# Performance work log

Measured on AMD Instinct MI355X. Metric: run time of the kernel, lower is better.

The kernel has to match this reference:

```python
import jax, jax.numpy as jnp
import numpy as np

B, N, T, E = 8, 10000, 12, 160000
C_IN, C_SP, C_OUT, K = 32, 64, 64, 3
EPS = 1e-5

def _conv1xk(x, w, b, pad):
    # x: (B, Cin, N, T), w: (Cout, Cin, 1, k) -- conv only along time axis
    y = jax.lax.conv_general_dilated(x, w, (1, 1), [(0, 0), (pad, pad)],
                                     dimension_numbers=('NCHW', 'OIHW', 'NCHW'))
    return y + b[None, :, None, None]

def _temporal_block(x, w, b, gamma, beta, mean, var):
    out = _conv1xk(x, w, b, pad=1)
    p, q = jnp.split(out, 2, axis=1)
    out = p * jax.nn.sigmoid(q)  # GLU gate
    scale = gamma * jax.lax.rsqrt(var + EPS)  # eval-mode BatchNorm2d
    return (out - mean[None, :, None, None]) * scale[None, :, None, None] + beta[None, :, None, None]

def _cheb_conv(x, edge_index, edge_weight, W, b):
    # x: (BT, N, C). PyG ChebConv, sym normalization, lambda_max=2 =>
    # Lhat = -D^{-1/2} A D^{-1/2} (zero diagonal). Recursion T0=x, T1=Lhat x,
    # Tk = 2 Lhat T_{k-1} - T_{k-2}; out = sum_k Tk @ W_k + b.
    row, col = edge_index[0], edge_index[1]
    n = x.shape[1]
    deg = jnp.zeros((n,), x.dtype).at[row].add(edge_weight)
    deg_safe = jnp.where(deg > 0, deg, 1.0)
    dinv = jnp.where(deg > 0, jax.lax.rsqrt(deg_safe), 0.0)
    norm = -edge_weight * dinv[row] * dinv[col]  # (E,)

    def lhat(z):
        msg = z[:, row, :] * norm[None, :, None]          # gather + scale
        return jnp.zeros_like(z).at[:, col, :].add(msg)   # scatter-add

    Tx0 = x
    out = jnp.einsum('bnc,cd->bnd', Tx0, W[0])
    Tx1 = lhat(x)
    out = out + jnp.einsum('bnc,cd->bnd', Tx1, W[1])
    for k in range(2, W.shape[0]):
        Tx2 = 2.0 * lhat(Tx1) - Tx0
        out = out + jnp.einsum('bnc,cd->bnd', Tx2, W[k])
        Tx0, Tx1 = Tx1, Tx2
    return out + b

def setup_inputs():
    key = jax.random.key(0)
    ks = jax.random.split(key, 16)
    s = 0.05
    return {
        'x': jax.random.normal(ks[0], (B, C_IN, N, T), jnp.float32),
        'edge_index': jax.random.randint(ks[1], (2, E), 0, N),
        'edge_weight': jax.random.uniform(ks[2], (E,), jnp.float32),
        'w_gate1': jax.random.normal(ks[3], (2 * C_SP, C_IN, 1, 3), jnp.float32) * s,
        'b_gate1': jnp.zeros((2 * C_SP,), jnp.float32),
        'bn1_gamma': 1.0 + 0.1 * jax.random.normal(ks[4], (C_SP,), jnp.float32),
        'bn1_beta': 0.1 * jax.random.normal(ks[5], (C_SP,), jnp.float32),
        'bn1_mean': 0.1 * jax.random.normal(ks[6], (C_SP,), jnp.float32),
        'bn1_var': jax.random.uniform(ks[7], (C_SP,), jnp.float32, 0.5, 1.5),
        'cheb_w': jax.random.normal(ks[8], (K, C_SP, C_SP), jnp.float32) * s,
        'cheb_b': jnp.zeros((C_SP,), jnp.float32),
        'ln_gamma': jnp.ones((C_SP,), jnp.float32),
        'ln_beta': jnp.zeros((C_SP,), jnp.float32),
        'w_gate2': jax.random.normal(ks[9], (2 * C_OUT, C_SP, 1, 3), jnp.float32) * s,
        'b_gate2': jnp.zeros((2 * C_OUT,), jnp.float32),
        'bn2_gamma': 1.0 + 0.1 * jax.random.normal(ks[10], (C_OUT,), jnp.float32),
        'bn2_beta': 0.1 * jax.random.normal(ks[11], (C_OUT,), jnp.float32),
        'bn2_mean': 0.1 * jax.random.normal(ks[12], (C_OUT,), jnp.float32),
        'bn2_var': jax.random.uniform(ks[13], (C_OUT,), jnp.float32, 0.5, 1.5),
        'w_res': jax.random.normal(ks[14], (C_OUT, C_IN, 1, 1), jnp.float32) * s,
        'b_res': jnp.zeros((C_OUT,), jnp.float32),
    }

def reference(x, edge_index, edge_weight, w_gate1, b_gate1, bn1_gamma, bn1_beta, bn1_mean, bn1_var,
              cheb_w, cheb_b, ln_gamma, ln_beta, w_gate2, b_gate2, bn2_gamma, bn2_beta, bn2_mean,
              bn2_var, w_res, b_res):
    b_, _, n_, t_ = x.shape
    res = _conv1xk(x, w_res, b_res, pad=0)  # 1x1 residual projection
    out = _temporal_block(x, w_gate1, b_gate1, bn1_gamma, bn1_beta, bn1_mean, bn1_var)
    c_s = out.shape[1]
    # (B, C_s, N, T) -> (B*T, N, C_s): spatial graph conv per time snapshot
    h = out.transpose(0, 3, 2, 1).reshape(b_ * t_, n_, c_s)
    h = _cheb_conv(h, edge_index, edge_weight, cheb_w, cheb_b)
    mu = h.mean(-1, keepdims=True)
    var = ((h - mu) ** 2).mean(-1, keepdims=True)
    h = (h - mu) * jax.lax.rsqrt(var + EPS) * ln_gamma + ln_beta  # LayerNorm
    h = jax.nn.relu(h)
    h = h.reshape(b_, t_, n_, c_s).transpose(0, 3, 2, 1)
    out = _temporal_block(h, w_gate2, b_gate2, bn2_gamma, bn2_beta, bn2_mean, bn2_var)
    return out + res
```

## Files before the change

### kernel.cpp

```cpp
#include <hip/hip_runtime.h>
#include <math.h>

#define BB 8
#define CIN 32
#define NN 10000
#define TTT 12
#define EE 160000
#define CSP 64
#define BT (BB*TTT)
#define EPSV 1e-5f

typedef __attribute__((ext_vector_type(8))) short bf16x8;
typedef __attribute__((ext_vector_type(4))) float f32x4;

static __device__ __forceinline__ float sigmoidf_(float v) {
    return __builtin_amdgcn_rcpf(1.f + __expf(-v));
}

static __device__ __forceinline__ short f2bf(float v) {
    unsigned u = __float_as_uint(v);
    u = (u + 0x7fffu + ((u >> 16) & 1u)) >> 16;
    return (short)u;
}
static __device__ __forceinline__ float lo16f(unsigned u) {
    return __uint_as_float(u << 16);
}
static __device__ __forceinline__ float hi16f(unsigned u) {
    return __uint_as_float(u & 0xffff0000u);
}
static __device__ __forceinline__ unsigned packbf(float a, float b) {
    return ((unsigned)(ushort)f2bf(a)) | (((unsigned)(ushort)f2bf(b)) << 16);
}

__global__ void k_deg(const int* __restrict__ ei, const float* __restrict__ ew,
                      float* __restrict__ deg) {
    int e = blockIdx.x * 256 + threadIdx.x;
    if (e < EE) atomicAdd(&deg[ei[e]], ew[e]);
}

__global__ void k_dinv(float* __restrict__ deg) {
    int n = blockIdx.x * 256 + threadIdx.x;
    if (n < NN) { float d = deg[n]; deg[n] = d > 0.f ? rsqrtf(d) : 0.f; }
}

__global__ void k_norm_cnt(const int* __restrict__ ei, const float* __restrict__ ew,
                           const float* __restrict__ dinv, float* __restrict__ nrm,
                           int* __restrict__ cnt) {
    int e = blockIdx.x * 256 + threadIdx.x;
    if (e < EE) {
        int r = ei[e], c = ei[EE + e];
        nrm[e] = -ew[e] * dinv[r] * dinv[c];
        atomicAdd(&cnt[c], 1);
    }
}

__global__ void k_scan(const int* __restrict__ cnt, int* __restrict__ offs,
                       int* __restrict__ cursor) {
    __shared__ int sh[1024];
    int tid = threadIdx.x;
    int running = 0;
    for (int base = 0; base < NN; base += 1024) {
        int i = base + tid;
        int v = (i < NN) ? cnt[i] : 0;
        sh[tid] = v;
        __syncthreads();
        for (int off = 1; off < 1024; off <<= 1) {
            int t = (tid >= off) ? sh[tid - off] : 0;
            __syncthreads();
            sh[tid] += t;
            __syncthreads();
        }
        int incl = sh[tid];
        if (i < NN) { offs[i] = running + incl - v; cursor[i] = running + incl - v; }
        int ct = sh[1023];
        __syncthreads();
        running += ct;
    }
    if (tid == 0) offs[NN] = running;
}

__global__ void k_fill(const int* __restrict__ ei, const float* __restrict__ nrm,
                       int* __restrict__ cursor, unsigned* __restrict__ csrp) {
    int e = blockIdx.x * 256 + threadIdx.x;
    if (e < EE) {
        int cdst = ei[EE + e];
        int p = atomicAdd(&cursor[cdst], 1);
        csrp[p] = (((unsigned)(ushort)f2bf(nrm[e])) << 16) | (unsigned)ei[e];
    }
}

__global__ void k_cvt_w(const float* __restrict__ wg1, const float* __restrict__ wg2,
                        const float* __restrict__ wr, const float* __restrict__ cwf,
                        short* __restrict__ o1, short* __restrict__ o2,
                        short* __restrict__ o3, short* __restrict__ wt02,
                        short* __restrict__ wt1, short* __restrict__ wt2) {
    int i = blockIdx.x * 256 + threadIdx.x;
    if (i < 12288) o1[i] = f2bf(wg1[i]);
    if (i < 24576) o2[i] = f2bf(wg2[i]);
    if (i < 2048)  o3[i] = f2bf(wr[i]);
    if (i < 4096) {
        int cout = i >> 6, cin = i & 63;
        float w0 = cwf[cin * 64 + cout];
        float w1 = cwf[4096 + cin * 64 + cout];
        float w2 = cwf[8192 + cin * 64 + cout];
        wt02[i] = f2bf(w0 - w2);
        wt1[i]  = f2bf(w1);
        wt2[i]  = f2bf(w2);
    }
}

__global__ __launch_bounds__(256, 4) void k_tconv1_mfma(
    const float* __restrict__ x, const short* __restrict__ wbf,
    const float* __restrict__ bg, const float* __restrict__ gam,
    const float* __restrict__ bet, const float* __restrict__ mean,
    const float* __restrict__ var, ushort* __restrict__ h1)
{
    __shared__ short Btl[3 * 48 * 40];
    int bi = blockIdx.x;
    int b = bi / 2500;
    int n0 = (bi % 2500) * 4;
    int tid = threadIdx.x;

    for (int j = tid; j < 384; j += 256) {
        int ci = j / 12, r = j - ci * 12;
        const float* xp = x + ((size_t)(b * CIN + ci) * NN + n0) * 12 + r * 4;
        float4 v = *(const float4*)xp;
        float vv[4] = {v.x, v.y, v.z, v.w};
#pragma unroll
        for (int e = 0; e < 4; ++e) {
            int at = r * 4 + e;
            int n = at / 12, t = at - n * 12;
            short bv = f2bf(vv[e]);
#pragma unroll
            for (int kk = 0; kk < 3; ++kk) {
                int tp = t + 1 - kk;
                if (tp >= 0 && tp < 12) {
                    int K = ci * 3 + kk;
                    Btl[((K >> 5) * 48 + n * 12 + tp) * 40 + (K & 31)] = bv;
                }
            }
            if (t == 0)  { int K = ci * 3;     Btl[((K >> 5) * 48 + n * 12) * 40 + (K & 31)] = 0; }
            if (t == 11) { int K = ci * 3 + 2; Btl[((K >> 5) * 48 + n * 12 + 11) * 40 + (K & 31)] = 0; }
        }
    }
    __syncthreads();

    int w = tid >> 6, l = tid & 63, lr = l & 15, lq = l >> 4;
    f32x4 aP[3], aQ[3];
#pragma unroll
    for (int m = 0; m < 3; ++m) { aP[m] = (f32x4){0,0,0,0}; aQ[m] = (f32x4){0,0,0,0}; }

#pragma unroll
    for (int ks = 0; ks < 3; ++ks) {
        bf16x8 wp = *(const bf16x8*)(wbf + ((w * 16 + lr) * 96 + ks * 32 + lq * 8));
        bf16x8 wq = *(const bf16x8*)(wbf + ((64 + w * 16 + lr) * 96 + ks * 32 + lq * 8));
#pragma unroll
        for (int mt = 0; mt < 3; ++mt) {
            bf16x8 im = *(const bf16x8*)(&Btl[(ks * 48 + mt * 16 + lr) * 40 + lq * 8]);
            aP[mt] = __builtin_amdgcn_mfma_f32_16x16x32_bf16(im, wp, aP[mt], 0, 0, 0);
            aQ[mt] = __builtin_amdgcn_mfma_f32_16x16x32_bf16(im, wq, aQ[mt], 0, 0, 0);
        }
    }

    int c = w * 16 + lr;
    float bp = bg[c], bq = bg[64 + c];
    float sc = gam[c] * rsqrtf(var[c] + EPSV);
    float mn = mean[c], be = bet[c];
#pragma unroll
    for (int mt = 0; mt < 3; ++mt) {
#pragma unroll
        for (int j = 0; j < 4; ++j) {
            int row = mt * 16 + lq * 4 + j;
            int n = n0 + row / 12, t = row % 12;
            float h = (aP[mt][j] + bp) * sigmoidf_(aQ[mt][j] + bq);
            h1[((size_t)(b * TTT + t) * NN + n) * 64 + c] = (ushort)f2bf((h - mn) * sc + be);
        }
    }
}

__global__ __launch_bounds__(256, 8) void k_spatial(
    const ushort* __restrict__ h1, const int* __restrict__ offs,
    const unsigned* __restrict__ csr,
    const short* __restrict__ wt02, const short* __restrict__ wt1,
    const short* __restrict__ wt2, const float* __restrict__ cb,
    ushort* __restrict__ O, ushort* __restrict__ U)
{
    __shared__ short Al[64][72];
    __shared__ short Gl[64][72];
    int tid = threadIdx.x;
    int bi = blockIdx.x;
    int xcd = bi & 7, r = bi >> 3;
    int jp = r / 313, ck = r - jp * 313;
    int bt0 = xcd * 12 + jp * 2;
    int n0 = ck * 32;

    const ushort* hb0 = h1 + (size_t)bt0 * NN * 64;
    const ushort* hb1 = hb0 + (size_t)NN * 64;
    int w = tid >> 6, l = tid & 63;
    int qw = l >> 4, cp = l & 15;
    int qs = w * 4 + qw;

#pragma unroll
    for (int p = 0; p < 2; ++p) {
        int nl = qs * 2 + p;
        int n = n0 + nl;
        float4 aa0 = {0,0,0,0}, ab0 = aa0, aa1 = aa0, ab1 = aa0;
        uint2 sv0 = {0u,0u}, sv1 = {0u,0u};
        if (n < NN) {
            sv0 = *(const uint2*)(hb0 + (size_t)n * 64 + cp * 4);
            sv1 = *(const uint2*)(hb1 + (size_t)n * 64 + cp * 4);
            int o0 = offs[n], o1 = offs[n + 1];
            int i = o0;
            for (; i + 3 < o1; i += 4) {
                unsigned e0 = csr[i], e1 = csr[i + 1], e2 = csr[i + 2], e3 = csr[i + 3];
                size_t x0 = (size_t)(e0 & 0xffffu) * 64 + cp * 4;
                size_t x1 = (size_t)(e1 & 0xffffu) * 64 + cp * 4;
                size_t x2 = (size_t)(e2 & 0xffffu) * 64 + cp * 4;
                size_t x3 = (size_t)(e3 & 0xffffu) * 64 + cp * 4;
                uint2 r00 = *(const uint2*)(hb0 + x0);
                uint2 r01 = *(const uint2*)(hb1 + x0);
                uint2 r10 = *(const uint2*)(hb0 + x1);
                uint2 r11 = *(const uint2*)(hb1 + x1);
                uint2 r20 = *(const uint2*)(hb0 + x2);
                uint2 r21 = *(const uint2*)(hb1 + x2);
                uint2 r30 = *(const uint2*)(hb0 + x3);
                uint2 r31 = *(const uint2*)(hb1 + x3);
                float w0 = hi16f(e0), w1 = hi16f(e1), w2 = hi16f(e2), w3 = hi16f(e3);
                aa0.x = fmaf(w0, lo16f(r00.x), aa0.x); aa0.y = fmaf(w0, hi16f(r00.x), aa0.y);
                aa0.z = fmaf(w0, lo16f(r00.y), aa0.z); aa0.w = fmaf(w0, hi16f(r00.y), aa0.w);
                ab0.x = fmaf(w1, lo16f(r10.x), ab0.x); ab0.y = fmaf(w1, hi16f(r10.x), ab0.y);
                ab0.z = fmaf(w1, lo16f(r10.y), ab0.z); ab0.w = fmaf(w1, hi16f(r10.y), ab0.w);
                aa0.x = fmaf(w2, lo16f(r20.x), aa0.x); aa0.y = fmaf(w2, hi16f(r20.x), aa0.y);
                aa0.z = fmaf(w2, lo16f(r20.y), aa0.z); aa0.w = fmaf(w2, hi16f(r20.y), aa0.w);
                ab0.x = fmaf(w3, lo16f(r30.x), ab0.x); ab0.y = fmaf(w3, hi16f(r30.x), ab0.y);
                ab0.z = fmaf(w3, lo16f(r30.y), ab0.z); ab0.w = fmaf(w3, hi16f(r30.y), ab0.w);
                aa1.x = fmaf(w0, lo16f(r01.x), aa1.x); aa1.y = fmaf(w0, hi16f(r01.x), aa1.y);
                aa1.z = fmaf(w0, lo16f(r01.y), aa1.z); aa1.w = fmaf(w0, hi16f(r01.y), aa1.w);
                ab1.x = fmaf(w1, lo16f(r11.x), ab1.x); ab1.y = fmaf(w1, hi16f(r11.x), ab1.y);
                ab1.z = fmaf(w1, lo16f(r11.y), ab1.z); ab1.w = fmaf(w1, hi16f(r11.y), ab1.w);
                aa1.x = fmaf(w2, lo16f(r21.x), aa1.x); aa1.y = fmaf(w2, hi16f(r21.x), aa1.y);
                aa1.z = fmaf(w2, lo16f(r21.y), aa1.z); aa1.w = fmaf(w2, hi16f(r21.y), aa1.w);
                ab1.x = fmaf(w3, lo16f(r31.x), ab1.x); ab1.y = fmaf(w3, hi16f(r31.x), ab1.y);
                ab1.z = fmaf(w3, lo16f(r31.y), ab1.z); ab1.w = fmaf(w3, hi16f(r31.y), ab1.w);
            }
            for (; i < o1; ++i) {
                unsigned e = csr[i];
                size_t xx = (size_t)(e & 0xffffu) * 64 + cp * 4;
                uint2 r0 = *(const uint2*)(hb0 + xx);
                uint2 r1 = *(const uint2*)(hb1 + xx);
                float ww = hi16f(e);
                aa0.x = fmaf(ww, lo16f(r0.x), aa0.x); aa0.y = fmaf(ww, hi16f(r0.x), aa0.y);
                aa0.z = fmaf(ww, lo16f(r0.y), aa0.z); aa0.w = fmaf(ww, hi16f(r0.y), aa0.w);
                aa1.x = fmaf(ww, lo16f(r1.x), aa1.x); aa1.y = fmaf(ww, hi16f(r1.x), aa1.y);
                aa1.z = fmaf(ww, lo16f(r1.y), aa1.z); aa1.w = fmaf(ww, hi16f(r1.y), aa1.w);
            }
        }
        *(uint2*)&Al[nl][cp * 4] = sv0;
        *(uint2*)&Al[32 + nl][cp * 4] = sv1;
        uint2 g0 = { packbf(aa0.x + ab0.x, aa0.y + ab0.y), packbf(aa0.z + ab0.z, aa0.w + ab0.w) };
        uint2 g1 = { packbf(aa1.x + ab1.x, aa1.y + ab1.y), packbf(aa1.z + ab1.z, aa1.w + ab1.w) };
        *(uint2*)&Gl[nl][cp * 4] = g0;
        *(uint2*)&Gl[32 + nl][cp * 4] = g1;
    }
    __syncthreads();

    int lr = l & 15, lq = l >> 4;
    bf16x8 af[2], gf[2];
#pragma unroll
    for (int ks = 0; ks < 2; ++ks) {
        af[ks] = *(const bf16x8*)&Al[w * 16 + lr][ks * 32 + lq * 8];
        gf[ks] = *(const bf16x8*)&Gl[w * 16 + lr][ks * 32 + lq * 8];
    }
    f32x4 ao[4], au[4];
#pragma unroll
    for (int ct = 0; ct < 4; ++ct) { ao[ct] = (f32x4){0,0,0,0}; au[ct] = (f32x4){0,0,0,0}; }
#pragma unroll
    for (int ct = 0; ct < 4; ++ct) {
#pragma unroll
        for (int ks = 0; ks < 2; ++ks) {
            int woff = (ct * 16 + lr) * 64 + ks * 32 + lq * 8;
            bf16x8 b02 = *(const bf16x8*)(wt02 + woff);
            bf16x8 b1  = *(const bf16x8*)(wt1 + woff);
            bf16x8 b2  = *(const bf16x8*)(wt2 + woff);
            ao[ct] = __builtin_amdgcn_mfma_f32_16x16x32_bf16(af[ks], b02, ao[ct], 0, 0, 0);
            ao[ct] = __builtin_amdgcn_mfma_f32_16x16x32_bf16(gf[ks], b1,  ao[ct], 0, 0, 0);
            au[ct] = __builtin_amdgcn_mfma_f32_16x16x32_bf16(gf[ks], b2,  au[ct], 0, 0, 0);
        }
    }
    __syncthreads();

#pragma unroll
    for (int ct = 0; ct < 4; ++ct) {
        float bb = cb[ct * 16 + lr];
#pragma unroll
        for (int j2 = 0; j2 < 4; ++j2) {
            int node = w * 16 + lq * 4 + j2;
            Al[node][ct * 16 + lr] = f2bf(ao[ct][j2] + bb);
            Gl[node][ct * 16 + lr] = f2bf(au[ct][j2]);
        }
    }
    __syncthreads();

    size_t obase = (size_t)bt0 * NN * 64;
#pragma unroll
    for (int rr = 0; rr < 2; ++rr) {
        int idx = tid + rr * 256;
        int row = idx >> 3, seg = idx & 7;
        int snap = row >> 5, nl2 = row & 31;
        int n = n0 + nl2;
        if (n < NN) {
            size_t off = obase + (size_t)snap * NN * 64 + (size_t)n * 64 + seg * 8;
            __builtin_nontemporal_store(*(const bf16x8*)&Al[row][seg * 8], (bf16x8*)(O + off));
            __builtin_nontemporal_store(*(const bf16x8*)&Gl[row][seg * 8], (bf16x8*)(U + off));
        }
    }
}

__global__ __launch_bounds__(256, 8) void k_gather2_ln(
    const ushort* __restrict__ O, const ushort* __restrict__ U,
    const int* __restrict__ offs, const unsigned* __restrict__ csr,
    const float* __restrict__ lng, const float* __restrict__ lnb,
    ushort* __restrict__ hln)
{
    int bi = blockIdx.x;
    int xcd = bi & 7, r = bi >> 3;
    int jp = r / 625, ck = r - jp * 625;
    int bt0 = xcd * 12 + jp * 2;
    int ng = ck * 16;
    int tid = threadIdx.x;
    int w = tid >> 6, l = tid & 63;
    int qw = l >> 4, cp = l & 15;
    int n = ng + w * 4 + qw;
    const ushort* Ub0 = U + (size_t)bt0 * NN * 64;
    const ushort* Ub1 = Ub0 + (size_t)NN * 64;
    size_t sidx0 = (size_t)bt0 * NN * 64 + (size_t)n * 64 + cp * 4;
    size_t sidx1 = sidx0 + (size_t)NN * 64;

    float4 aa0 = {0,0,0,0}, ab0 = aa0, aa1 = aa0, ab1 = aa0;
    int o0 = offs[n], o1 = offs[n + 1];
    int i = o0;
    for (; i + 3 < o1; i += 4) {
        unsigned e0 = csr[i], e1 = csr[i + 1], e2 = csr[i + 2], e3 = csr[i + 3];
        size_t x0 = (size_t)(e0 & 0xffffu) * 64 + cp * 4;
        size_t x1 = (size_t)(e1 & 0xffffu) * 64 + cp * 4;
        size_t x2 = (size_t)(e2 & 0xffffu) * 64 + cp * 4;
        size_t x3 = (size_t)(e3 & 0xffffu) * 64 + cp * 4;
        uint2 r00 = *(const uint2*)(Ub0 + x0);
        uint2 r01 = *(const uint2*)(Ub1 + x0);
        uint2 r10 = *(const uint2*)(Ub0 + x1);
        uint2 r11 = *(const uint2*)(Ub1 + x1);
        uint2 r20 = *(const uint2*)(Ub0 + x2);
        uint2 r21 = *(const uint2*)(Ub1 + x2);
        uint2 r30 = *(const uint2*)(Ub0 + x3);
        uint2 r31 = *(const uint2*)(Ub1 + x3);
        float w0 = hi16f(e0), w1 = hi16f(e1), w2 = hi16f(e2), w3 = hi16f(e3);
        aa0.x = fmaf(w0, lo16f(r00.x), aa0.x); aa0.y = fmaf(w0, hi16f(r00.x), aa0.y);
        aa0.z = fmaf(w0, lo16f(r00.y), aa0.z); aa0.w = fmaf(w0, hi16f(r00.y), aa0.w);
        ab0.x = fmaf(w1, lo16f(r10.x), ab0.x); ab0.y = fmaf(w1, hi16f(r10.x), ab0.y);
        ab0.z = fmaf(w1, lo16f(r10.y), ab0.z); ab0.w = fmaf(w1, hi16f(r10.y), ab0.w);
        aa0.x = fmaf(w2, lo16f(r20.x), aa0.x); aa0.y = fmaf(w2, hi16f(r20.x), aa0.y);
        aa0.z = fmaf(w2, lo16f(r20.y), aa0.z); aa0.w = fmaf(w2, hi16f(r20.y), aa0.w);
        ab0.x = fmaf(w3, lo16f(r30.x), ab0.x); ab0.y = fmaf(w3, hi16f(r30.x), ab0.y);
        ab0.z = fmaf(w3, lo16f(r30.y), ab0.z); ab0.w = fmaf(w3, hi16f(r30.y), ab0.w);
        aa1.x = fmaf(w0, lo16f(r01.x), aa1.x); aa1.y = fmaf(w0, hi16f(r01.x), aa1.y);
        aa1.z = fmaf(w0, lo16f(r01.y), aa1.z); aa1.w = fmaf(w0, hi16f(r01.y), aa1.w);
        ab1.x = fmaf(w1, lo16f(r11.x), ab1.x); ab1.y = fmaf(w1, hi16f(r11.x), ab1.y);
        ab1.z = fmaf(w1, lo16f(r11.y), ab1.z); ab1.w = fmaf(w1, hi16f(r11.y), ab1.w);
        aa1.x = fmaf(w2, lo16f(r21.x), aa1.x); aa1.y = fmaf(w2, hi16f(r21.x), aa1.y);
        aa1.z = fmaf(w2, lo16f(r21.y), aa1.z); aa1.w = fmaf(w2, hi16f(r21.y), aa1.w);
        ab1.x = fmaf(w3, lo16f(r31.x), ab1.x); ab1.y = fmaf(w3, hi16f(r31.x), ab1.y);
        ab1.z = fmaf(w3, lo16f(r31.y), ab1.z); ab1.w = fmaf(w3, hi16f(r31.y), ab1.w);
    }
    for (; i < o1; ++i) {
        unsigned e = csr[i];
        size_t xx = (size_t)(e & 0xffffu) * 64 + cp * 4;
        uint2 r0 = *(const uint2*)(Ub0 + xx);
        uint2 r1 = *(const uint2*)(Ub1 + xx);
        float ww = hi16f(e);
        aa0.x = fmaf(ww, lo16f(r0.x), aa0.x); aa0.y = fmaf(ww, hi16f(r0.x), aa0.y);
        aa0.z = fmaf(ww, lo16f(r0.y), aa0.z); aa0.w = fmaf(ww, hi16f(r0.y), aa0.w);
        aa1.x = fmaf(ww, lo16f(r1.x), aa1.x); aa1.y = fmaf(ww, hi16f(r1.x), aa1.y);
        aa1.z = fmaf(ww, lo16f(r1.y), aa1.z); aa1.w = fmaf(ww, hi16f(r1.y), aa1.w);
    }

    float4 g = *(const float4*)(lng + cp * 4);
    float4 be = *(const float4*)(lnb + cp * 4);
#pragma unroll
    for (int s = 0; s < 2; ++s) {
        size_t sidx = s ? sidx1 : sidx0;
        float4 aa = s ? aa1 : aa0;
        float4 ab = s ? ab1 : ab0;
        uint2 ov = *(const uint2*)(O + sidx);
        float acc0 = lo16f(ov.x) + 2.f * (aa.x + ab.x);
        float acc1 = hi16f(ov.x) + 2.f * (aa.y + ab.y);
        float acc2 = lo16f(ov.y) + 2.f * (aa.z + ab.z);
        float acc3 = hi16f(ov.y) + 2.f * (aa.w + ab.w);
        float s1 = (acc0 + acc1) + (acc2 + acc3);
        float s2 = (acc0 * acc0 + acc1 * acc1) + (acc2 * acc2 + acc3 * acc3);
#pragma unroll
        for (int m = 8; m >= 1; m >>= 1) {
            s1 += __shfl_xor(s1, m);
            s2 += __shfl_xor(s2, m);
        }
        float mu = s1 * (1.f / 64.f);
        float vr = s2 * (1.f / 64.f) - mu * mu;
        float rstd = rsqrtf(vr + EPSV);
        float y0 = fmaxf((acc0 - mu) * rstd * g.x + be.x, 0.f);
        float y1 = fmaxf((acc1 - mu) * rstd * g.y + be.y, 0.f);
        float y2 = fmaxf((acc2 - mu) * rstd * g.z + be.z, 0.f);
        float y3 = fmaxf((acc3 - mu) * rstd * g.w + be.w, 0.f);
        uint2 pk = { packbf(y0, y1), packbf(y2, y3) };
        __builtin_nontemporal_store(*(unsigned long long*)&pk,
                                    (unsigned long long*)(hln + sidx));
    }
}

__global__ __launch_bounds__(256, 4) void k_tconv2_mfma(
    const ushort* __restrict__ hln, const float* __restrict__ x,
    const short* __restrict__ wbf, const short* __restrict__ wrbf,
    const float* __restrict__ bg, const float* __restrict__ gam,
    const float* __restrict__ bet, const float* __restrict__ mean,
    const float* __restrict__ var, const float* __restrict__ bres,
    float* __restrict__ out)
{
    __shared__ short Btl[6 * 48 * 40];
    __shared__ short Bx[48 * 40];
    int bi = blockIdx.x;
    int b = bi / 2500;
    int n0 = (bi % 2500) * 4;
    int tid = threadIdx.x;

    {
        int n = tid >> 6, c = tid & 63;
#pragma unroll
        for (int t = 0; t < 12; ++t) {
            short bv = (short)hln[((size_t)(b * TTT + t) * NN + n0 + n) * 64 + c];
#pragma unroll
            for (int kk = 0; kk < 3; ++kk) {
                int tp = t + 1 - kk;
                if (tp >= 0 && tp < 12) {
                    int K = c * 3 + kk;
                    Btl[((K >> 5) * 48 + n * 12 + tp) * 40 + (K & 31)] = bv;
                }
            }
            if (t == 0)  { int K = c * 3;     Btl[((K >> 5) * 48 + n * 12) * 40 + (K & 31)] = 0; }
            if (t == 11) { int K = c * 3 + 2; Btl[((K >> 5) * 48 + n * 12 + 11) * 40 + (K & 31)] = 0; }
        }
    }
    for (int j = tid; j < 384; j += 256) {
        int ci = j / 12, r = j - ci * 12;
        const float* xp = x + ((size_t)(b * CIN + ci) * NN + n0) * 12 + r * 4;
        float4 v = *(const float4*)xp;
        float vv[4] = {v.x, v.y, v.z, v.w};
#pragma unroll
        for (int e = 0; e < 4; ++e) {
            int col = r * 4 + e;
            Bx[col * 40 + ci] = f2bf(vv[e]);
        }
    }
    __syncthreads();

    int w = tid >> 6, l = tid & 63, lr = l & 15, lq = l >> 4;
    f32x4 accP[3], accQ[3], accR[3];
#pragma unroll
    for (int m = 0; m < 3; ++m) {
        accP[m] = (f32x4){0,0,0,0}; accQ[m] = (f32x4){0,0,0,0}; accR[m] = (f32x4){0,0,0,0};
    }

#pragma unroll
    for (int ks = 0; ks < 6; ++ks) {
        bf16x8 aP = *(const bf16x8*)(wbf + ((w * 16 + lr) * 192 + ks * 32 + lq * 8));
        bf16x8 aQ = *(const bf16x8*)(wbf + ((64 + w * 16 + lr) * 192 + ks * 32 + lq * 8));
#pragma unroll
        for (int ct = 0; ct < 3; ++ct) {
            bf16x8 bfr = *(const bf16x8*)(&Btl[(ks * 48 + ct * 16 + lr) * 40 + lq * 8]);
            accP[ct] = __builtin_amdgcn_mfma_f32_16x16x32_bf16(aP, bfr, accP[ct], 0, 0, 0);
            accQ[ct] = __builtin_amdgcn_mfma_f32_16x16x32_bf16(aQ, bfr, accQ[ct], 0, 0, 0);
        }
    }
    {
        bf16x8 aR = *(const bf16x8*)(wrbf + ((w * 16 + lr) * 32 + lq * 8));
#pragma unroll
        for (int ct = 0; ct < 3; ++ct) {
            bf16x8 bx = *(const bf16x8*)(&Bx[(ct * 16 + lr) * 40 + lq * 8]);
            accR[ct] = __builtin_amdgcn_mfma_f32_16x16x32_bf16(aR, bx, accR[ct], 0, 0, 0);
        }
    }

    float bpv[4], bqv[4], scv[4], mnv[4], bev[4], brv[4];
#pragma unroll
    for (int j = 0; j < 4; ++j) {
        int cj = w * 16 + lq * 4 + j;
        bpv[j] = bg[cj]; bqv[j] = bg[64 + cj];
        scv[j] = gam[cj] * rsqrtf(var[cj] + EPSV);
        mnv[j] = mean[cj]; bev[j] = bet[cj]; brv[j] = bres[cj];
    }
#pragma unroll
    for (int ct = 0; ct < 3; ++ct) {
        int col = ct * 16 + lr;
        int n = n0 + col / 12, t = col % 12;
#pragma unroll
        for (int j = 0; j < 4; ++j) {
            int cj = w * 16 + lq * 4 + j;
            float h = (accP[ct][j] + bpv[j]) * sigmoidf_(accQ[ct][j] + bqv[j]);
            float o = (h - mnv[j]) * scv[j] + bev[j] + accR[ct][j] + brv[j];
            __builtin_nontemporal_store(o, &out[((size_t)(b * 64 + cj) * NN + n) * 12 + t]);
        }
    }
}

extern "C" void kernel_launch(void* const* d_in, const int* in_sizes, int n_in,
                              void* d_out, int out_size, void* d_ws, size_t ws_size,
                              hipStream_t stream)
{
    const float* x   = (const float*)d_in[0];
    const int*   ei  = (const int*)d_in[1];
    const float* ew  = (const float*)d_in[2];
    const float* wg1 = (const float*)d_in[3];
    const float* bg1 = (const float*)d_in[4];
    const float* g1  = (const float*)d_in[5];
    const float* be1 = (const float*)d_in[6];
    const float* m1  = (const float*)d_in[7];
    const float* v1  = (const float*)d_in[8];
    const float* cw  = (const float*)d_in[9];
    const float* cb  = (const float*)d_in[10];
    const float* lng = (const float*)d_in[11];
    const float* lnb = (const float*)d_in[12];
    const float* wg2 = (const float*)d_in[13];
    const float* bg2 = (const float*)d_in[14];
    const float* g2  = (const float*)d_in[15];
    const float* be2 = (const float*)d_in[16];
    const float* m2  = (const float*)d_in[17];
    const float* v2  = (const float*)d_in[18];
    const float* wr  = (const float*)d_in[19];
    const float* br  = (const float*)d_in[20];

    char* w = (char*)d_ws;
    short* wbf1  = (short*)w;  w += 12288 * 2;
    short* wbf2  = (short*)w;  w += 24576 * 2;
    short* wrbf  = (short*)w;  w += 2048 * 2;
    short* wt02  = (short*)w;  w += 4096 * 2;
    short* wt1   = (short*)w;  w += 4096 * 2;
    short* wt2   = (short*)w;  w += 4096 * 2;
    ushort* h1   = (ushort*)w; w += (size_t)BT * NN * 64 * 2;
    ushort* O    = (ushort*)w; w += (size_t)BT * NN * 64 * 2;
    float* deg   = (float*)w;  w += NN * 4;
    int*   cnt   = (int*)w;    w += NN * 4;
    int*   offs  = (int*)w;    w += (NN + 1) * 4;
    int*   cursor= (int*)w;    w += NN * 4;
    float* nrm   = (float*)w;  w += EE * 4;
    unsigned* csr = (unsigned*)w; w += EE * 4;
    ushort* U = (ushort*)d_out;

    hipMemsetAsync(deg, 0, NN * 4 * 2, stream);

    k_deg<<<625, 256, 0, stream>>>(ei, ew, deg);
    k_dinv<<<40, 256, 0, stream>>>(deg);
    k_norm_cnt<<<625, 256, 0, stream>>>(ei, ew, deg, nrm, cnt);
    k_scan<<<1, 1024, 0, stream>>>(cnt, offs, cursor);
    k_fill<<<625, 256, 0, stream>>>(ei, nrm, cursor, csr);
    k_cvt_w<<<96, 256, 0, stream>>>(wg1, wg2, wr, cw, wbf1, wbf2, wrbf, wt02, wt1, wt2);

    k_tconv1_mfma<<<BB * 2500, 256, 0, stream>>>(x, wbf1, bg1, g1, be1, m1, v1, h1);
    k_spatial<<<8 * 6 * 313, 256, 0, stream>>>(h1, offs, csr, wt02, wt1, wt2, cb, O, U);
    k_gather2_ln<<<8 * 6 * 625, 256, 0, stream>>>(O, U, offs, csr, lng, lnb, h1);
    k_tconv2_mfma<<<BB * 2500, 256, 0, stream>>>(h1, x, wbf2, wrbf, bg2, g2, be2, m2, v2, br,
                                                 (float*)d_out);
}
```

Before: 960.0 us.

## Interleave snapshot pairs per node so gathers fetch 256-byte contiguous rows

Intermediate activations (h1, O, U, hln) change from a [bt][node][64] layout to [pair][node][2 snapshots x 64], so one neighbour gather reads one contiguous 256-byte row for both snapshots. Each wavefront now handles one node, with lanes covering both snapshots and 2 channels each, and loads 4-byte elements instead of two separate 8-byte loads from different snapshot planes. CSR offsets are made wave-uniform with readfirstlane. The intent is fewer, better-coalesced memory transactions in the sparse gather, at the cost of changed indexing in the producer and consumer kernels and smaller per-lane loads.

After: 894.8 us. 1.07x faster.

```diff
diff --git a/kernel.cpp b/kernel.cpp
--- a/kernel.cpp
+++ b/kernel.cpp
@@ -8,6 +8,7 @@
 #define EE 160000
 #define CSP 64
 #define BT (BB*TTT)
+#define NPAIR 48
 #define EPSV 1e-5f
 
 typedef __attribute__((ext_vector_type(8))) short bf16x8;
@@ -173,7 +174,8 @@
             int row = mt * 16 + lq * 4 + j;
             int n = n0 + row / 12, t = row % 12;
             float h = (aP[mt][j] + bp) * sigmoidf_(aQ[mt][j] + bq);
-            h1[((size_t)(b * TTT + t) * NN + n) * 64 + c] = (ushort)f2bf((h - mn) * sc + be);
+            h1[((size_t)(b * 6 + (t >> 1)) * NN + n) * 128 + (t & 1) * 64 + c] =
+                (ushort)f2bf((h - mn) * sc + be);
         }
     }
 }
@@ -191,76 +193,47 @@
     int bi = blockIdx.x;
     int xcd = bi & 7, r = bi >> 3;
     int jp = r / 313, ck = r - jp * 313;
-    int bt0 = xcd * 12 + jp * 2;
+    int pair = xcd * 6 + jp;
     int n0 = ck * 32;
 
-    const ushort* hb0 = h1 + (size_t)bt0 * NN * 64;
-    const ushort* hb1 = hb0 + (size_t)NN * 64;
+    const char* hp = (const char*)h1 + (size_t)pair * NN * 256;
     int w = tid >> 6, l = tid & 63;
-    int qw = l >> 4, cp = l & 15;
-    int qs = w * 4 + qw;
-
-#pragma unroll
-    for (int p = 0; p < 2; ++p) {
-        int nl = qs * 2 + p;
+    int snap = l >> 5, cp = l & 31;
+    unsigned loff = (unsigned)(snap * 128 + cp * 4);
+
+#pragma unroll
+    for (int p = 0; p < 8; ++p) {
+        int nl = p * 4 + w;
         int n = n0 + nl;
-        float4 aa0 = {0,0,0,0}, ab0 = aa0, aa1 = aa0, ab1 = aa0;
-        uint2 sv0 = {0u,0u}, sv1 = {0u,0u};
+        float a0 = 0.f, a1 = 0.f, b0 = 0.f, b1 = 0.f;
+        unsigned sv = 0;
         if (n < NN) {
-            sv0 = *(const uint2*)(hb0 + (size_t)n * 64 + cp * 4);
-            sv1 = *(const uint2*)(hb1 + (size_t)n * 64 + cp * 4);
-            int o0 = offs[n], o1 = offs[n + 1];
+            sv = *(const unsigned*)(hp + (((unsigned)n) << 8) + loff);
+            int o0 = __builtin_amdgcn_readfirstlane(offs[n]);
+            int o1 = __builtin_amdgcn_readfirstlane(offs[n + 1]);
             int i = o0;
             for (; i + 3 < o1; i += 4) {
                 unsigned e0 = csr[i], e1 = csr[i + 1], e2 = csr[i + 2], e3 = csr[i + 3];
-                size_t x0 = (size_t)(e0 & 0xffffu) * 64 + cp * 4;
-                size_t x1 = (size_t)(e1 & 0xffffu) * 64 + cp * 4;
-                size_t x2 = (size_t)(e2 & 0xffffu) * 64 + cp * 4;
-                size_t x3 = (size_t)(e3 & 0xffffu) * 64 + cp * 4;
-                uint2 r00 = *(const uint2*)(hb0 + x0);
-                uint2 r01 = *(const uint2*)(hb1 + x0);
-                uint2 r10 = *(const uint2*)(hb0 + x1);
-                uint2 r11 = *(const uint2*)(hb1 + x1);
-                uint2 r20 = *(const uint2*)(hb0 + x2);
-                uint2 r21 = *(const uint2*)(hb1 + x2);
-                uint2 r30 = *(const uint2*)(hb0 + x3);
-                uint2 r31 = *(const uint2*)(hb1 + x3);
+                unsigned r0 = *(const unsigned*)(hp + ((e0 & 0xffffu) << 8) + loff);
+                unsigned r1 = *(const unsigned*)(hp + ((e1 & 0xffffu) << 8) + loff);
+                unsigned r2 = *(const unsigned*)(hp + ((e2 & 0xffffu) << 8) + loff);
+                unsigned r3 = *(const unsigned*)(hp + ((e3 & 0xffffu) << 8) + loff);
                 float w0 = hi16f(e0), w1 = hi16f(e1), w2 = hi16f(e2), w3 = hi16f(e3);
-                aa0.x = fmaf(w0, lo16f(r00.x), aa0.x); aa0.y = fmaf(w0, hi16f(r00.x), aa0.y);
-                aa0.z = fmaf(w0, lo16f(r00.y), aa0.z); aa0.w = fmaf(w0, hi16f(r00.y), aa0.w);
-                ab0.x = fmaf(w1, lo16f(r10.x), ab0.x); ab0.y = fmaf(w1, hi16f(r10.x), ab0.y);
-                ab0.z = fmaf(w1, lo16f(r10.y), ab0.z); ab0.w = fmaf(w1, hi16f(r10.y), ab0.w);
-                aa0.x = fmaf(w2, lo16f(r20.x), aa0.x); aa0.y = fmaf(w2, hi16f(r20.x), aa0.y);
-                aa0.z = fmaf(w2, lo16f(r20.y), aa0.z); aa0.w = fmaf(w2, hi16f(r20.y), aa0.w);
-                ab0.x = fmaf(w3, lo16f(r30.x), ab0.x); ab0.y = fmaf(w3, hi16f(r30.x), ab0.y);
-                ab0.z = fmaf(w3, lo16f(r30.y), ab0.z); ab0.w = fmaf(w3, hi16f(r30.y), ab0.w);
-                aa1.x = fmaf(w0, lo16f(r01.x), aa1.x); aa1.y = fmaf(w0, hi16f(r01.x), aa1.y);
-                aa1.z = fmaf(w0, lo16f(r01.y), aa1.z); aa1.w = fmaf(w0, hi16f(r01.y), aa1.w);
-                ab1.x = fmaf(w1, lo16f(r11.x), ab1.x); ab1.y = fmaf(w1, hi16f(r11.x), ab1.y);
-                ab1.z = fmaf(w1, lo16f(r11.y), ab1.z); ab1.w = fmaf(w1, hi16f(r11.y), ab1.w);
-                aa1.x = fmaf(w2, lo16f(r21.x), aa1.x); aa1.y = fmaf(w2, hi16f(r21.x), aa1.y);
-                aa1.z = fmaf(w2, lo16f(r21.y), aa1.z); aa1.w = fmaf(w2, hi16f(r21.y), aa1.w);
-                ab1.x = fmaf(w3, lo16f(r31.x), ab1.x); ab1.y = fmaf(w3, hi16f(r31.x), ab1.y);
-                ab1.z = fmaf(w3, lo16f(r31.y), ab1.z); ab1.w = fmaf(w3, hi16f(r31.y), ab1.w);
+                a0 = fmaf(w0, lo16f(r0), a0); a1 = fmaf(w0, hi16f(r0), a1);
+                b0 = fmaf(w1, lo16f(r1), b0); b1 = fmaf(w1, hi16f(r1), b1);
+                a0 = fmaf(w2, lo16f(r2), a0); a1 = fmaf(w2, hi16f(r2), a1);
+                b0 = fmaf(w3, lo16f(r3), b0); b1 = fmaf(w3, hi16f(r3), b1);
             }
             for (; i < o1; ++i) {
                 unsigned e = csr[i];
-                size_t xx = (size_t)(e & 0xffffu) * 64 + cp * 4;
-                uint2 r0 = *(const uint2*)(hb0 + xx);
-                uint2 r1 = *(const uint2*)(hb1 + xx);
+                unsigned rr = *(const unsigned*)(hp + ((e & 0xffffu) << 8) + loff);
                 float ww = hi16f(e);
-                aa0.x = fmaf(ww, lo16f(r0.x), aa0.x); aa0.y = fmaf(ww, hi16f(r0.x), aa0.y);
-                aa0.z = fmaf(ww, lo16f(r0.y), aa0.z); aa0.w = fmaf(ww, hi16f(r0.y), aa0.w);
-                aa1.x = fmaf(ww, lo16f(r1.x), aa1.x); aa1.y = fmaf(ww, hi16f(r1.x), aa1.y);
-                aa1.z = fmaf(ww, lo16f(r1.y), aa1.z); aa1.w = fmaf(ww, hi16f(r1.y), aa1.w);
+                a0 = fmaf(ww, lo16f(rr), a0); a1 = fmaf(ww, hi16f(rr), a1);
             }
         }
-        *(uint2*)&Al[nl][cp * 4] = sv0;
-        *(uint2*)&Al[32 + nl][cp * 4] = sv1;
-        uint2 g0 = { packbf(aa0.x + ab0.x, aa0.y + ab0.y), packbf(aa0.z + ab0.z, aa0.w + ab0.w) };
-        uint2 g1 = { packbf(aa1.x + ab1.x, aa1.y + ab1.y), packbf(aa1.z + ab1.z, aa1.w + ab1.w) };
-        *(uint2*)&Gl[nl][cp * 4] = g0;
-        *(uint2*)&Gl[32 + nl][cp * 4] = g1;
+        int row = snap * 32 + nl;
+        *(unsigned*)&Al[row][cp * 2] = sv;
+        *(unsigned*)&Gl[row][cp * 2] = packbf(a0 + b0, a1 + b1);
     }
     __syncthreads();
 
@@ -294,24 +267,26 @@
         float bb = cb[ct * 16 + lr];
 #pragma unroll
         for (int j2 = 0; j2 < 4; ++j2) {
-            int node = w * 16 + lq * 4 + j2;
-            Al[node][ct * 16 + lr] = f2bf(ao[ct][j2] + bb);
-            Gl[node][ct * 16 + lr] = f2bf(au[ct][j2]);
+            int rowo = w * 16 + lq * 4 + j2;
+            Al[rowo][ct * 16 + lr] = f2bf(ao[ct][j2] + bb);
+            Gl[rowo][ct * 16 + lr] = f2bf(au[ct][j2]);
         }
     }
     __syncthreads();
 
-    size_t obase = (size_t)bt0 * NN * 64;
+    size_t obase = (size_t)pair * NN * 128;
 #pragma unroll
     for (int rr = 0; rr < 2; ++rr) {
         int idx = tid + rr * 256;
-        int row = idx >> 3, seg = idx & 7;
-        int snap = row >> 5, nl2 = row & 31;
-        int n = n0 + nl2;
+        int node = idx >> 4, part = idx & 15;
+        int sn = part >> 3, seg = part & 7;
+        int n = n0 + node;
         if (n < NN) {
-            size_t off = obase + (size_t)snap * NN * 64 + (size_t)n * 64 + seg * 8;
-            __builtin_nontemporal_store(*(const bf16x8*)&Al[row][seg * 8], (bf16x8*)(O + off));
-            __builtin_nontemporal_store(*(const bf16x8*)&Gl[row][seg * 8], (bf16x8*)(U + off));
+            size_t off = obase + (size_t)n * 128 + sn * 64 + seg * 8;
+            __builtin_nontemporal_store(*(const bf16x8*)&Al[sn * 32 + node][seg * 8],
+                                        (bf16x8*)(O + off));
+            __builtin_nontemporal_store(*(const bf16x8*)&Gl[sn * 32 + node][seg * 8],
+                                        (bf16x8*)(U + off));
         }
     }
 }
@@ -325,93 +300,61 @@
     int bi = blockIdx.x;
     int xcd = bi & 7, r = bi >> 3;
     int jp = r / 625, ck = r - jp * 625;
-    int bt0 = xcd * 12 + jp * 2;
+    int pair = xcd * 6 + jp;
     int ng = ck * 16;
     int tid = threadIdx.x;
     int w = tid >> 6, l = tid & 63;
-    int qw = l >> 4, cp = l & 15;
-    int n = ng + w * 4 + qw;
-    const ushort* Ub0 = U + (size_t)bt0 * NN * 64;
-    const ushort* Ub1 = Ub0 + (size_t)NN * 64;
-    size_t sidx0 = (size_t)bt0 * NN * 64 + (size_t)n * 64 + cp * 4;
-    size_t sidx1 = sidx0 + (size_t)NN * 64;
-
-    float4 aa0 = {0,0,0,0}, ab0 = aa0, aa1 = aa0, ab1 = aa0;
-    int o0 = offs[n], o1 = offs[n + 1];
-    int i = o0;
-    for (; i + 3 < o1; i += 4) {
-        unsigned e0 = csr[i], e1 = csr[i + 1], e2 = csr[i + 2], e3 = csr[i + 3];
-        size_t x0 = (size_t)(e0 & 0xffffu) * 64 + cp * 4;
-        size_t x1 = (size_t)(e1 & 0xffffu) * 64 + cp * 4;
-        size_t x2 = (size_t)(e2 & 0xffffu) * 64 + cp * 4;
-        size_t x3 = (size_t)(e3 & 0xffffu) * 64 + cp * 4;
-        uint2 r00 = *(const uint2*)(Ub0 + x0);
-        uint2 r01 = *(const uint2*)(Ub1 + x0);
-        uint2 r10 = *(const uint2*)(Ub0 + x1);
-        uint2 r11 = *(const uint2*)(Ub1 + x1);
-        uint2 r20 = *(const uint2*)(Ub0 + x2);
-        uint2 r21 = *(const uint2*)(Ub1 + x2);
-        uint2 r30 = *(const uint2*)(Ub0 + x3);
-        uint2 r31 = *(const uint2*)(Ub1 + x3);
-        float w0 = hi16f(e0), w1 = hi16f(e1), w2 = hi16f(e2), w3 = hi16f(e3);
-        aa0.x = fmaf(w0, lo16f(r00.x), aa0.x); aa0.y = fmaf(w0, hi16f(r00.x), aa0.y);
-        aa0.z = fmaf(w0, lo16f(r00.y), aa0.z); aa0.w = fmaf(w0, hi16f(r00.y), aa0.w);
-        ab0.x = fmaf(w1, lo16f(r10.x), ab0.x); ab0.y = fmaf(w1, hi16f(r10.x), ab0.y);
-        ab0.z = fmaf(w1, lo16f(r10.y), ab0.z); ab0.w = fmaf(w1, hi16f(r10.y), ab0.w);
-        aa0.x = fmaf(w2, lo16f(r20.x), aa0.x); aa0.y = fmaf(w2, hi16f(r20.x), aa0.y);
-        aa0.z = fmaf(w2, lo16f(r20.y), aa0.z); aa0.w = fmaf(w2, hi16f(r20.y), aa0.w);
-        ab0.x = fmaf(w3, lo16f(r30.x), ab0.x); ab0.y = fmaf(w3, hi16f(r30.x), ab0.y);
-        ab0.z = fmaf(w3, lo16f(r30.y), ab0.z); ab0.w = fmaf(w3, hi16f(r30.y), ab0.w);
-        aa1.x = fmaf(w0, lo16f(r01.x), aa1.x); aa1.y = fmaf(w0, hi16f(r01.x), aa1.y);
-        aa1.z = fmaf(w0, lo16f(r01.y), aa1.z); aa1.w = fmaf(w0, hi16f(r01.y), aa1.w);
-        ab1.x = fmaf(w1, lo16f(r11.x), ab1.x); ab1.y = fmaf(w1, hi16f(r11.x), ab1.y);
-        ab1.z = fmaf(w1, lo16f(r11.y), ab1.z); ab1.w = fmaf(w1, hi16f(r11.y), ab1.w);
-        aa1.x = fmaf(w2, lo16f(r21.x), aa1.x); aa1.y = fmaf(w2, hi16f(r21.x), aa1.y);
-        aa1.z = fmaf(w2, lo16f(r21.y), aa1.z); aa1.w = fmaf(w2, hi16f(r21.y), aa1.w);
-        ab1.x = fmaf(w3, lo16f(r31.x), ab1.x); ab1.y = fmaf(w3, hi16f(r31.x), ab1.y);
-        ab1.z = fmaf(w3, lo16f(r31.y), ab1.z); ab1.w = fmaf(w3, hi16f(r31.y), ab1.w);
-    }
-    for (; i < o1; ++i) {
-        unsigned e = csr[i];
-        size_t xx = (size_t)(e & 0xffffu) * 64 + cp * 4;
-        uint2 r0 = *(const uint2*)(Ub0 + xx);
-        uint2 r1 = *(const uint2*)(Ub1 + xx);
-        float ww = hi16f(e);
-        aa0.x = fmaf(ww, lo16f(r0.x), aa0.x); aa0.y = fmaf(ww, hi16f(r0.x), aa0.y);
-        aa0.z = fmaf(ww, lo16f(r0.y), aa0.z); aa0.w = fmaf(ww, hi16f(r0.y), aa0.w);
-        aa1.x = fmaf(ww, lo16f(r1.x), aa1.x); aa1.y = fmaf(ww, hi16f(r1.x), aa1.y);
-        aa1.z = fmaf(ww, lo16f(r1.y), aa1.z); aa1.w = fmaf(ww, hi16f(r1.y), aa1.w);
-    }
-
-    float4 g = *(const float4*)(lng + cp * 4);
-    float4 be = *(const float4*)(lnb + cp * 4);
-#pragma unroll
-    for (int s = 0; s < 2; ++s) {
-        size_t sidx = s ? sidx1 : sidx0;
-        float4 aa = s ? aa1 : aa0;
-        float4 ab = s ? ab1 : ab0;
-        uint2 ov = *(const uint2*)(O + sidx);
-        float acc0 = lo16f(ov.x) + 2.f * (aa.x + ab.x);
-        float acc1 = hi16f(ov.x) + 2.f * (aa.y + ab.y);
-        float acc2 = lo16f(ov.y) + 2.f * (aa.z + ab.z);
-        float acc3 = hi16f(ov.y) + 2.f * (aa.w + ab.w);
-        float s1 = (acc0 + acc1) + (acc2 + acc3);
-        float s2 = (acc0 * acc0 + acc1 * acc1) + (acc2 * acc2 + acc3 * acc3);
-#pragma unroll
-        for (int m = 8; m >= 1; m >>= 1) {
+    int snap = l >> 5, cp = l & 31;
+    unsigned loff = (unsigned)(snap * 128 + cp * 4);
+    const char* up = (const char*)U + (size_t)pair * NN * 256;
+    const char* op = (const char*)O + (size_t)pair * NN * 256;
+    ushort* hlp = hln + (size_t)pair * NN * 128;
+
+    float2 gv = ((const float2*)lng)[cp];
+    float2 bv = ((const float2*)lnb)[cp];
+
+#pragma unroll
+    for (int p = 0; p < 4; ++p) {
+        int n = ng + p * 4 + w;
+        float a0 = 0.f, a1 = 0.f, b0 = 0.f, b1 = 0.f;
+        int o0 = __builtin_amdgcn_readfirstlane(offs[n]);
+        int o1 = __builtin_amdgcn_readfirstlane(offs[n + 1]);
+        int i = o0;
+        for (; i + 3 < o1; i += 4) {
+            unsigned e0 = csr[i], e1 = csr[i + 1], e2 = csr[i + 2], e3 = csr[i + 3];
+            unsigned r0 = *(const unsigned*)(up + ((e0 & 0xffffu) << 8) + loff);
+            unsigned r1 = *(const unsigned*)(up + ((e1 & 0xffffu) << 8) + loff);
+            unsigned r2 = *(const unsigned*)(up + ((e2 & 0xffffu) << 8) + loff);
+            unsigned r3 = *(const unsigned*)(up + ((e3 & 0xffffu) << 8) + loff);
+            float w0 = hi16f(e0), w1 = hi16f(e1), w2 = hi16f(e2), w3 = hi16f(e3);
+            a0 = fmaf(w0, lo16f(r0), a0); a1 = fmaf(w0, hi16f(r0), a1);
+            b0 = fmaf(w1, lo16f(r1), b0); b1 = fmaf(w1, hi16f(r1), b1);
+            a0 = fmaf(w2, lo16f(r2), a0); a1 = fmaf(w2, hi16f(r2), a1);
+            b0 = fmaf(w3, lo16f(r3), b0); b1 = fmaf(w3, hi16f(r3), b1);
+        }
+        for (; i < o1; ++i) {
+            unsigned e = csr[i];
+            unsigned rr = *(const unsigned*)(up + ((e & 0xffffu) << 8) + loff);
+            float ww = hi16f(e);
+            a0 = fmaf(ww, lo16f(rr), a0); a1 = fmaf(ww, hi16f(rr), a1);
+        }
+        unsigned ov = *(const unsigned*)(op + (((unsigned)n) << 8) + loff);
+        float acc0 = lo16f(ov) + 2.f * (a0 + b0);
+        float acc1 = hi16f(ov) + 2.f * (a1 + b1);
+        float s1 = acc0 + acc1;
+        float s2 = acc0 * acc0 + acc1 * acc1;
+#pragma unroll
+        for (int m = 16; m >= 1; m >>= 1) {
             s1 += __shfl_xor(s1, m);
             s2 += __shfl_xor(s2, m);
         }
         float mu = s1 * (1.f / 64.f);
         float vr = s2 * (1.f / 64.f) - mu * mu;
         float rstd = rsqrtf(vr + EPSV);
-        float y0 = fmaxf((acc0 - mu) * rstd * g.x + be.x, 0.f);
-        float y1 = fmaxf((acc1 - mu) * rstd * g.y + be.y, 0.f);
-        float y2 = fmaxf((acc2 - mu) * rstd * g.z + be.z, 0.f);
-        float y3 = fmaxf((acc3 - mu) * rstd * g.w + be.w, 0.f);
-        uint2 pk = { packbf(y0, y1), packbf(y2, y3) };
-        __builtin_nontemporal_store(*(unsigned long long*)&pk,
-                                    (unsigned long long*)(hln + sidx));
+        float y0 = fmaxf((acc0 - mu) * rstd * gv.x + bv.x, 0.f);
+        float y1 = fmaxf((acc1 - mu) * rstd * gv.y + bv.y, 0.f);
+        __builtin_nontemporal_store(packbf(y0, y1),
+            (unsigned*)(hlp + (size_t)n * 128 + snap * 64 + cp * 2));
     }
 }
 
@@ -434,7 +377,8 @@
         int n = tid >> 6, c = tid & 63;
 #pragma unroll
         for (int t = 0; t < 12; ++t) {
-            short bv = (short)hln[((size_t)(b * TTT + t) * NN + n0 + n) * 64 + c];
+            short bv = (short)hln[((size_t)(b * 6 + (t >> 1)) * NN + n0 + n) * 128 +
+                                  (t & 1) * 64 + c];
 #pragma unroll
             for (int kk = 0; kk < 3; ++kk) {
                 int tp = t + 1 - kk;
@@ -542,8 +486,8 @@
     short* wt02  = (short*)w;  w += 4096 * 2;
     short* wt1   = (short*)w;  w += 4096 * 2;
     short* wt2   = (short*)w;  w += 4096 * 2;
-    ushort* h1   = (ushort*)w; w += (size_t)BT * NN * 64 * 2;
-    ushort* O    = (ushort*)w; w += (size_t)BT * NN * 64 * 2;
+    ushort* h1   = (ushort*)w; w += (size_t)NPAIR * NN * 128 * 2;
+    ushort* O    = (ushort*)w; w += (size_t)NPAIR * NN * 128 * 2;
     float* deg   = (float*)w;  w += NN * 4;
     int*   cnt   = (int*)w;    w += NN * 4;
     int*   offs  = (int*)w;    w += (NN + 1) * 4;
```
